# Kernel optimization log

Hardware: AMD Instinct MI355X
Metric: run time of the kernel (lower is better)

## Reference

```python
import jax, jax.numpy as jnp
import numpy as np
from jax import lax

V, E, H, B, S, T = 50000, 256, 512, 16, 400, 100
MAX_OOV, UNK, LAMB = 100, 1, 1.0
NEG = -1e30


def gru_scan(xs, h0, Wih, Whh, bih, bhh):
    """xs: (S,B,E), h0: (B,H) -> (hs (S,B,H), hT (B,H)). PyTorch GRU cell math."""
    gi_all = xs @ Wih.T + bih  # (S,B,3H) precomputed input projections
    def step(h, gi):
        gh = h @ Whh.T + bhh
        r = jax.nn.sigmoid(gi[..., :H] + gh[..., :H])
        z = jax.nn.sigmoid(gi[..., H:2 * H] + gh[..., H:2 * H])
        n = jnp.tanh(gi[..., 2 * H:] + r * gh[..., 2 * H:])
        hn = (1.0 - z) * n + z * h
        return hn, hn
    hT, hs = lax.scan(step, h0, gi_all)
    return hs, hT


def gru_cell(x, h, Wih, Whh, bih, bhh):
    gi = x @ Wih.T + bih
    gh = h @ Whh.T + bhh
    r = jax.nn.sigmoid(gi[..., :H] + gh[..., :H])
    z = jax.nn.sigmoid(gi[..., H:2 * H] + gh[..., H:2 * H])
    n = jnp.tanh(gi[..., 2 * H:] + r * gh[..., 2 * H:])
    return (1.0 - z) * n + z * h


def pgn_forward(floats, src_vecs, tgt_vecs, max_oov):
    (src_mask, enc_embed, dec_embed,
     eWih_f, eWhh_f, ebih_f, ebhh_f, eWih_b, eWhh_b, ebih_b, ebhh_b,
     dWih, dWhh, dbih, dbhh,
     aWh, abh, aWs, abs_, aWc, abc, aV, abv,
     rW, rb, gW, gb, fW, fb) = floats

    # --- encoder (bidirectional GRU) ---
    src_in = jnp.where(src_vecs >= V, UNK, src_vecs)          # replace_oov
    xs = enc_embed[src_in].transpose(1, 0, 2)                  # (S,B,E)
    h0 = jnp.zeros((B, H), xs.dtype)
    hs_f, hT_f = gru_scan(xs, h0, eWih_f, eWhh_f, ebih_f, ebhh_f)
    hs_b, hT_b = gru_scan(xs[::-1], h0, eWih_b, eWhh_b, ebih_b, ebhh_b)
    enc_out = jnp.concatenate([hs_f, hs_b[::-1]], -1).transpose(1, 0, 2)  # (B,S,2H)
    enc_hidden = jnp.concatenate([hT_f, hT_b], -1)             # (B,2H)

    # reducer: initial decoder hidden (torch names it context_vec)
    h_dec0 = enc_hidden @ rW.T + rb                            # (B,H)

    # precompute Wh(enc_output) once (loop-invariant)
    Wh_enc = jnp.einsum('bsd,hd->bsh', enc_out, aWh) + abh     # (B,S,H)
    mask_s = src_mask[..., 0] > 0                              # (B,S)
    wc_vec = aWc[:, 0]                                         # (H,)
    rows = jnp.arange(B)

    dec_in = jnp.where(tgt_vecs[:, :-1] >= V, UNK, tgt_vecs[:, :-1]).T  # (T-1,B)
    targets = tgt_vecs[:, 1:].T                                          # (T-1,B)

    def step(carry, inp):
        h, cov = carry                      # (B,H), (B,S)
        tok, tgt_t = inp
        x = dec_embed[tok]                  # (B,E)
        hdec = gru_cell(x, h, dWih, dWhh, dbih, dbhh)          # (B,H)
        # Bahdanau attention with coverage
        s_part = hdec @ aWs.T + abs_                            # (B,H)
        c_part = cov[:, :, None] * wc_vec[None, None, :] + abc  # (B,S,H)
        e = jnp.tanh(Wh_enc + s_part[:, None, :] + c_part) @ aV[0] + abv[0]  # (B,S)
        attn = jax.nn.softmax(jnp.where(mask_s, e, NEG), axis=1)
        ctx = jnp.einsum('bs,bsd->bd', attn, enc_out)           # (B,2H)
        cov_new = cov + attn
        ctx_red = ctx @ rW.T + rb                               # (B,H)
        logits = jnp.concatenate([ctx_red, hdec], -1) @ fW.T + fb
        p_vocab = jax.nn.softmax(logits, -1)                    # (B,V)
        score = jnp.concatenate([ctx_red, hdec, x], -1) @ gW.T + gb  # (B,1)
        p_gen = jnp.clip(jax.nn.sigmoid(score), 0.001, 0.999)
        p_ext = jnp.concatenate(
            [p_gen * p_vocab, jnp.zeros((B, max_oov), p_vocab.dtype)], 1)
        p_ext = p_ext.at[rows[:, None], src_vecs].add((1.0 - p_gen) * attn)
        tp = p_ext[rows, tgt_t]
        cov_loss = jnp.sum(jnp.minimum(attn, cov_new), axis=1)
        loss = (-jnp.log(tp + 1e-9) + LAMB * cov_loss) * (tgt_t != 0).astype(tp.dtype)
        return (ctx_red, cov_new), loss

    cov0 = jnp.zeros((B, S), enc_out.dtype)
    _, losses = lax.scan(step, (h_dec0, cov0), (dec_in, targets))  # (T-1,B)
    batch_loss = losses.sum(0)
    tgt_lens = jnp.sum((tgt_vecs != 0).astype(batch_loss.dtype), axis=1) - 1.0
    return jnp.mean(batch_loss / tgt_lens)


def setup_inputs() -> dict:
    key = jax.random.key(0)
    ks = iter(jax.random.split(key, 40))
    def p(shape):
        return 0.02 * jax.random.normal(next(ks), shape, dtype=jnp.float32)
    def z(n):
        return jnp.zeros((n,), jnp.float32)
    inp = {
        'src_vecs': jax.random.randint(next(ks), (B, S), 0, V + MAX_OOV),
        'src_mask': jnp.ones((B, S, 1), jnp.float32),
        'tgt_vecs': jax.random.randint(next(ks), (B, T), 0, V),
        'max_oov': MAX_OOV,
        'enc_embed': p((V, E)), 'dec_embed': p((V, E)),
        'eWih_f': p((3 * H, E)), 'eWhh_f': p((3 * H, H)), 'ebih_f': z(3 * H), 'ebhh_f': z(3 * H),
        'eWih_b': p((3 * H, E)), 'eWhh_b': p((3 * H, H)), 'ebih_b': z(3 * H), 'ebhh_b': z(3 * H),
        'dWih': p((3 * H, E)), 'dWhh': p((3 * H, H)), 'dbih': z(3 * H), 'dbhh': z(3 * H),
        'aWh': p((H, 2 * H)), 'abh': z(H), 'aWs': p((H, H)), 'abs_': z(H),
        'aWc': p((H, 1)), 'abc': z(H), 'aV': p((1, H)), 'abv': z(1),
        'rW': p((H, 2 * H)), 'rb': z(H),
        'gW': p((1, 2 * H + E)), 'gb': z(1),
        'fW': p((V, 2 * H)), 'fb': z(V),
    }
    return inp


def reference(src_vecs, src_mask, tgt_vecs, max_oov, enc_embed, dec_embed,
              eWih_f, eWhh_f, ebih_f, ebhh_f, eWih_b, eWhh_b, ebih_b, ebhh_b,
              dWih, dWhh, dbih, dbhh,
              aWh, abh, aWs, abs_, aWc, abc, aV, abv,
              rW, rb, gW, gb, fW, fb):
    floats = (src_mask, enc_embed, dec_embed,
              eWih_f, eWhh_f, ebih_f, ebhh_f, eWih_b, eWhh_b, ebih_b, ebhh_b,
              dWih, dWhh, dbih, dbhh,
              aWh, abh, aWs, abs_, aWc, abc, aV, abv,
              rW, rb, gW, gb, fW, fb)
    return pgn_forward(floats, src_vecs, tgt_vecs, max_oov)
```

## Files before the change

### kernel.cpp

```cpp
#include <hip/hip_runtime.h>

#define V_SZ 50000
#define E_SZ 256
#define H_SZ 512
#define B_SZ 16
#define S_SZ 400
#define T_SZ 100
#define UNK_TOK 1
#define NEGV -1e30f

typedef unsigned short u16;
typedef unsigned int u32;
typedef __attribute__((ext_vector_type(8))) short sv8;
typedef __attribute__((ext_vector_type(4))) float f32x4;

__device__ __forceinline__ float bf2f(u16 u){ return __uint_as_float(((u32)u)<<16); }
__device__ __forceinline__ u16 f2bf(float x){
  u32 u = __float_as_uint(x);
  u32 r = (u + 0x7fffu + ((u>>16)&1u)) >> 16;
  return (u16)r;
}
__device__ __forceinline__ float wsum(float v){
  #pragma unroll
  for (int o=32;o;o>>=1) v += __shfl_xor(v,o);
  return v;
}
__device__ __forceinline__ float wmaxf(float v){
  #pragma unroll
  for (int o=32;o;o>>=1) v = fmaxf(v, __shfl_xor(v,o));
  return v;
}
__device__ __forceinline__ float ftanh(float x){
  float y = fminf(18.f, fmaxf(-18.f, 2.f*x));
  float e = __expf(y);
  return (e-1.f)/(e+1.f);
}
__device__ __forceinline__ float sigf(float x){ return 1.f/(1.f+__expf(-x)); }

__global__ void k_init(u32* h_bf, int* flags, float* cov, float* loss_acc){
  int idx = blockIdx.x*256 + threadIdx.x;
  if (idx < 16384) h_bf[idx] = 0u;
  if (idx < 1024) flags[idx] = 0;
  if (idx < B_SZ*S_SZ) cov[idx] = 0.f;
  if (idx < B_SZ) loss_acc[idx] = 0.f;
}

__global__ void k_transpose(const float* __restrict__ in, float* __restrict__ out, int R, int C){
  __shared__ float t[32][33];
  int c0 = blockIdx.x*32, r0 = blockIdx.y*32;
  int x = threadIdx.x, y = threadIdx.y;
  for (int j=y;j<32;j+=8){
    int r=r0+j, c=c0+x;
    t[j][x] = (r<R && c<C) ? in[r*C+c] : 0.f;
  }
  __syncthreads();
  for (int j=y;j<32;j+=8){
    int oc = c0+j, orr = r0+x;
    if (oc<C && orr<R) out[oc*R+orr] = t[x][j];
  }
}
__global__ void k_f2bf(const float* __restrict__ in, u16* __restrict__ out, int n){
  for (int i = blockIdx.x*256 + threadIdx.x; i < n; i += gridDim.x*256) out[i] = f2bf(in[i]);
}
__global__ void k_prep_frag(const float* __restrict__ W, u16* __restrict__ out, int Nt, int K32, int K){
  int idx = blockIdx.x*256 + threadIdx.x;
  if (idx >= Nt*K32*64) return;
  int lane = idx & 63; int kk = (idx>>6) % K32; int tile = idx / (K32*64);
  const float* src = W + (size_t)(tile*16 + (lane&15))*K + kk*32 + ((lane>>4)<<3);
  u16* dst = out + (size_t)idx*8;
  #pragma unroll
  for (int j=0;j<8;++j) dst[j] = f2bf(src[j]);
}

__global__ void k_gather_src(const int* __restrict__ src, const float* __restrict__ emb, float* __restrict__ xs){
  const int n = S_SZ*B_SZ*E_SZ;
  for (int idx = blockIdx.x*blockDim.x + threadIdx.x; idx < n; idx += gridDim.x*blockDim.x){
    int e = idx & 255; int sb = idx >> 8; int b = sb & 15; int s = sb >> 4;
    int tok = src[b*S_SZ + s]; if (tok >= V_SZ) tok = UNK_TOK;
    xs[idx] = emb[tok*E_SZ + e];
  }
}
__global__ void k_gather_dec(const int* __restrict__ tgt, const float* __restrict__ emb, float* __restrict__ dx){
  const int n = (T_SZ-1)*B_SZ*E_SZ;
  for (int idx = blockIdx.x*blockDim.x + threadIdx.x; idx < n; idx += gridDim.x*blockDim.x){
    int e = idx & 255; int tb = idx >> 8; int b = tb & 15; int t = tb >> 4;
    int tok = tgt[b*T_SZ + t]; if (tok >= V_SZ) tok = UNK_TOK;
    dx[idx] = emb[tok*E_SZ + e];
  }
}
__global__ void k_gxscore(const float* __restrict__ dx, const float* __restrict__ gW, float* __restrict__ gx){
  int i = blockIdx.x*blockDim.x + threadIdx.x;
  if (i < (T_SZ-1)*B_SZ){
    const float* x = dx + i*E_SZ;
    const float* g = gW + 1024;
    float a = 0.f;
    for (int e=0;e<E_SZ;++e) a += x[e]*g[e];
    gx[i] = a;
  }
}

__global__ __launch_bounds__(256) void k_gemm(const float* __restrict__ A, const float* __restrict__ WT,
                       const float* __restrict__ bias, float* __restrict__ C,
                       int M, int N, int K){
  __shared__ float As[32][36];
  int n = blockIdx.x*64 + (threadIdx.x & 63);
  int wv = threadIdx.x >> 6;
  int m0 = blockIdx.y*32;
  float acc[8];
  #pragma unroll
  for (int j=0;j<8;++j) acc[j]=0.f;
  for (int k0=0;k0<K;k0+=32){
    for (int e=threadIdx.x; e<1024; e+=256){
      int r = e>>5, c = e&31;
      int m = m0 + r;
      As[c][r] = (m<M)? A[m*K + k0 + c] : 0.f;
    }
    __syncthreads();
    #pragma unroll 8
    for (int k=0;k<32;++k){
      float w = WT[(k0+k)*N + n];
      const float* as = &As[k][wv*8];
      #pragma unroll
      for (int j=0;j<8;++j) acc[j] += as[j]*w;
    }
    __syncthreads();
  }
  float bv = bias[n];
  #pragma unroll
  for (int j=0;j<8;++j){
    int m = m0 + wv*8 + j;
    if (m<M) C[m*N + n] = acc[j] + bv;
  }
}

__global__ __launch_bounds__(64) void k_enc_persist(
    const float* __restrict__ gi_f, const float* __restrict__ gi_b,
    const u16* __restrict__ Wbf_f, const u16* __restrict__ Wbf_b,
    const float* __restrict__ bhh_f, const float* __restrict__ bhh_b,
    float* __restrict__ enc_out, float* __restrict__ enc_hid,
    u16* __restrict__ h_bf, int* __restrict__ flags){
  __shared__ u16 wl[48*512];
  int lane = threadIdx.x;
  int d = blockIdx.x >> 5, slice = blockIdx.x & 31;
  int h0 = slice*16;
  const u16* Wb = d ? Wbf_b : Wbf_f;
  const float* gi = d ? gi_b : gi_f;
  const float* bhh = d ? bhh_b : bhh_f;
  int hl = h0 + (lane & 15);
  int quad = lane >> 4;
  int* myflag = flags + (d*32 + slice)*16;
  int* pollp  = flags + (d*32 + (lane & 31))*16;

  #pragma unroll 4
  for (int i=0;i<48;++i){
    int gg = i>>4, kk = i&15;
    const u16* src = Wb + ((size_t)(gg*512 + hl))*512 + kk*32 + quad*8;
    *(sv8*)&wl[i*512 + lane*8] = *(const sv8*)src;
  }
  __syncthreads();

  float b0 = bhh[hl], b1 = bhh[512+hl], b2 = bhh[1024+hl];
  float hold[4] = {0.f,0.f,0.f,0.f};

  #pragma unroll 1
  for (int t=0;t<S_SZ;++t){
    int pos = d ? (S_SZ-1-t) : t;
    const float* gp = gi + ((size_t)pos*16)*1536 + hl;
    float giv[12];
    #pragma unroll
    for (int gg=0;gg<3;++gg)
      #pragma unroll
      for (int r=0;r<4;++r)
        giv[gg*4+r] = gp[(quad*4 + r)*1536 + gg*512];

    if (t > 0){
      while (true){
        int v = __hip_atomic_load(pollp, __ATOMIC_RELAXED, __HIP_MEMORY_SCOPE_AGENT);
        unsigned long long m = __ballot(v >= t);
        if (m == ~0ull) break;
        __builtin_amdgcn_s_sleep(1);
      }
      __threadfence();
    }

    const u16* hb = h_bf + ((size_t)(t&1)*2 + d)*8192 + (lane&15)*512 + quad*8;
    f32x4 a0={0.f,0.f,0.f,0.f}, a1={0.f,0.f,0.f,0.f}, a2={0.f,0.f,0.f,0.f};
    #pragma unroll
    for (int kk=0;kk<16;++kk){
      sv8 a = *(const sv8*)(hb + kk*32);
      a0 = __builtin_amdgcn_mfma_f32_16x16x32_bf16(a, *(const sv8*)&wl[(kk)*512 + lane*8], a0, 0,0,0);
      a1 = __builtin_amdgcn_mfma_f32_16x16x32_bf16(a, *(const sv8*)&wl[(16+kk)*512 + lane*8], a1, 0,0,0);
      a2 = __builtin_amdgcn_mfma_f32_16x16x32_bf16(a, *(const sv8*)&wl[(32+kk)*512 + lane*8], a2, 0,0,0);
    }
    u16* hw = h_bf + ((size_t)((t+1)&1)*2 + d)*8192;
    #pragma unroll
    for (int r=0;r<4;++r){
      int b = quad*4 + r;
      float rg = sigf(giv[r]   + a0[r] + b0);
      float zg = sigf(giv[4+r] + a1[r] + b1);
      float ng = ftanh(giv[8+r] + rg*(a2[r] + b2));
      float hv = (1.f-zg)*ng + zg*hold[r];
      hold[r] = hv;
      enc_out[((size_t)b*S_SZ + pos)*1024 + d*512 + hl] = hv;
      hw[b*512 + hl] = f2bf(hv);
      if (t == S_SZ-1) enc_hid[b*1024 + d*512 + hl] = hv;
    }
    __threadfence();
    if (lane == 0)
      __hip_atomic_store(myflag, t+1, __ATOMIC_RELEASE, __HIP_MEMORY_SCOPE_AGENT);
  }
}

__global__ __launch_bounds__(64) void k_dec_mfma(
    const float* __restrict__ dec_gi, u16* __restrict__ u_bf,
    const u16* __restrict__ dfrag, const float* __restrict__ bhh,
    float* __restrict__ hdec, int t){
  int slice = blockIdx.x; int lane = threadIdx.x; int quad = lane >> 4;
  int h = slice*16 + (lane & 15);
  const u16* ap = u_bf + (lane&15)*1024 + quad*8;
  f32x4 a0={0.f,0.f,0.f,0.f}, a1=a0, a2=a0;
  #pragma unroll
  for (int kk=0;kk<16;++kk){
    sv8 a = *(const sv8*)(ap + kk*32);
    a0 = __builtin_amdgcn_mfma_f32_16x16x32_bf16(a, *(const sv8*)(dfrag + ((size_t)(0*32+slice)*16 + kk)*512 + lane*8), a0, 0,0,0);
    a1 = __builtin_amdgcn_mfma_f32_16x16x32_bf16(a, *(const sv8*)(dfrag + ((size_t)(1*32+slice)*16 + kk)*512 + lane*8), a1, 0,0,0);
    a2 = __builtin_amdgcn_mfma_f32_16x16x32_bf16(a, *(const sv8*)(dfrag + ((size_t)(2*32+slice)*16 + kk)*512 + lane*8), a2, 0,0,0);
  }
  float b0 = bhh[h], b1 = bhh[512+h], b2 = bhh[1024+h];
  const float* gi = dec_gi + (size_t)t*16*1536 + h;
  #pragma unroll
  for (int r=0;r<4;++r){
    int b = quad*4 + r;
    const float* gb_ = gi + b*1536;
    float hlv = bf2f(u_bf[b*1024 + h]);
    float rg = sigf(gb_[0]    + a0[r] + b0);
    float zg = sigf(gb_[512]  + a1[r] + b1);
    float ng = ftanh(gb_[1024] + rg*(a2[r] + b2));
    float hv = (1.f-zg)*ng + zg*hlv;
    hdec[b*512 + h] = hv;
    u_bf[b*1024 + 512 + h] = f2bf(hv);
  }
}

__global__ __launch_bounds__(64) void k_spart_mfma(
    const u16* __restrict__ u_bf, const u16* __restrict__ sfrag,
    const float* __restrict__ abs_, float* __restrict__ s_part){
  int slice = blockIdx.x; int lane = threadIdx.x; int quad = lane >> 4;
  const u16* ap = u_bf + (lane&15)*1024 + 512 + quad*8;
  const u16* bp = sfrag + (size_t)slice*16*512 + lane*8;
  f32x4 acc={0.f,0.f,0.f,0.f};
  #pragma unroll
  for (int kk=0;kk<16;++kk){
    sv8 a = *(const sv8*)(ap + kk*32);
    acc = __builtin_amdgcn_mfma_f32_16x16x32_bf16(a, *(const sv8*)(bp + kk*512), acc, 0,0,0);
  }
  int h = slice*16 + (lane & 15);
  float bv = abs_[h];
  #pragma unroll
  for (int r=0;r<4;++r) s_part[(quad*4+r)*512 + h] = acc[r] + bv;
}

__global__ __launch_bounds__(512) void k_escore(
    const float* __restrict__ WhEnc, const float* __restrict__ s_part,
    const float* __restrict__ cov, const float* __restrict__ aWc,
    const float* __restrict__ abc, const float* __restrict__ aV,
    const float* __restrict__ abv, const float* __restrict__ mask,
    float* __restrict__ e_buf){
  int b = blockIdx.x >> 3; int s0 = (blockIdx.x & 7)*50;
  int tid = threadIdx.x, lane = tid & 63, w = tid >> 6;
  __shared__ float sp[512], wc[512], ab[512], av[512];
  sp[tid] = s_part[b*H_SZ + tid];
  wc[tid] = aWc[tid];
  ab[tid] = abc[tid];
  av[tid] = aV[tid];
  __syncthreads();
  float abv0 = abv[0];
  for (int s = s0 + w; s < s0+50; s += 8){
    float cv = cov[b*S_SZ + s];
    const float* wh = WhEnc + (b*S_SZ + s)*H_SZ;
    float a = 0.f;
    #pragma unroll
    for (int j=0;j<8;++j){
      int h = j*64 + lane;
      a += ftanh(wh[h] + sp[h] + cv*wc[h] + ab[h]) * av[h];
    }
    a = wsum(a);
    if (lane == 0){
      float e = a + abv0;
      if (!(mask[b*S_SZ + s] > 0.f)) e = NEGV;
      e_buf[b*S_SZ + s] = e;
    }
  }
}

__global__ __launch_bounds__(512) void k_attn_soft(
    const float* __restrict__ e_buf, float* __restrict__ attn,
    float* __restrict__ cov, float* __restrict__ covloss){
  int b = blockIdx.x; int tid = threadIdx.x, lane = tid & 63, w = tid >> 6;
  __shared__ float red[16];
  float e = (tid < S_SZ) ? e_buf[b*S_SZ + tid] : NEGV;
  float m = wmaxf(e);
  if (lane==0) red[w] = m;
  __syncthreads();
  if (tid < 64){
    float x = (lane < 8) ? red[lane] : NEGV;
    x = wmaxf(x);
    if (lane==0) red[8] = x;
  }
  __syncthreads();
  float mx = red[8];
  float pv = (tid < S_SZ) ? __expf(e - mx) : 0.f;
  float sm = wsum(pv);
  if (lane==0) red[w] = sm;
  __syncthreads();
  if (tid < 64){
    float x = (lane<8)? red[lane] : 0.f;
    x = wsum(x);
    if (lane==0) red[9] = x;
  }
  __syncthreads();
  float inv = 1.f/red[9];
  float ml = 0.f;
  if (tid < S_SZ){
    float a = pv*inv;
    attn[b*S_SZ+tid] = a;
    float cn = cov[b*S_SZ+tid] + a;
    cov[b*S_SZ+tid] = cn;
    ml = fminf(a, cn);
  }
  __syncthreads();
  float cs = wsum(ml);
  if (lane==0) red[w] = cs;
  __syncthreads();
  if (tid==0){
    float tot=0.f;
    for (int i=0;i<8;++i) tot += red[i];
    covloss[b] = tot;
  }
}

__global__ __launch_bounds__(128) void k_ctx(
    const float* __restrict__ attn, const float* __restrict__ enc_out,
    float* __restrict__ ctx){
  int b = blockIdx.x >> 3; int d0 = (blockIdx.x & 7)*128;
  int tid = threadIdx.x;
  float a = 0.f;
  const float* ao = attn + b*S_SZ;
  const float* eo = enc_out + b*S_SZ*1024 + d0 + tid;
  for (int s=0;s<S_SZ;++s) a += ao[s]*eo[s*1024];
  ctx[b*1024 + d0 + tid] = a;
}

__global__ __launch_bounds__(256) void k_ctxred(const float* __restrict__ ctx, const float* __restrict__ rWT,
    const float* __restrict__ rb, float* __restrict__ h_cur, u16* __restrict__ u_bf){
  __shared__ float As[64][17];
  int lane = threadIdx.x & 63, wv = threadIdx.x >> 6;
  int n = blockIdx.x*64 + lane;
  float acc[4] = {0.f,0.f,0.f,0.f};
  for (int k0=0;k0<1024;k0+=64){
    for (int e=threadIdx.x; e<1024; e+=256){
      int r = e & 15, c = e >> 4;
      As[c][r] = ctx[r*1024 + k0 + c];
    }
    __syncthreads();
    #pragma unroll 8
    for (int k=0;k<64;++k){
      float w = rWT[(k0+k)*512 + n];
      #pragma unroll
      for (int j=0;j<4;++j) acc[j] += As[k][wv*4+j]*w;
    }
    __syncthreads();
  }
  float bv = rb[n];
  #pragma unroll
  for (int j=0;j<4;++j){
    int m = wv*4+j;
    float val = acc[j] + bv;
    h_cur[m*512 + n] = val;
    u_bf[m*1024 + n] = f2bf(val);
  }
}

__global__ __launch_bounds__(256) void k_logits_mfma(
    const u16* __restrict__ u_bf, const u16* __restrict__ fwB,
    const float* __restrict__ fb, const int* __restrict__ tgt,
    float* __restrict__ se_part, float* __restrict__ logit_tgt, int t){
  int tid = threadIdx.x, lane = tid & 63, wv = tid >> 6;
  int tile = blockIdx.x*4 + wv;
  bool valid = tile < 3125;
  f32x4 acc = {0.f,0.f,0.f,0.f};
  if (valid){
    const u16* bp = fwB + (size_t)tile*16384 + lane*8;
    const u16* ap = u_bf + (lane&15)*1024 + (lane>>4)*8;
    #pragma unroll 8
    for (int kk=0;kk<32;++kk){
      sv8 a = *(const sv8*)(ap + kk*32);
      sv8 bfr = *(const sv8*)(bp + kk*512);
      acc = __builtin_amdgcn_mfma_f32_16x16x32_bf16(a, bfr, acc, 0,0,0);
    }
  }
  int v = tile*16 + (lane&15);
  float fbv = valid ? fb[v] : 0.f;
  float es0[4];
  #pragma unroll
  for (int r=0;r<4;++r){
    int b = (lane>>4)*4 + r;
    float lg = acc[r] + fbv;
    if (valid && v == tgt[b*T_SZ + t + 1]) logit_tgt[b] = lg;
    es0[r] = valid ? __expf(lg) : 0.f;
  }
  #pragma unroll
  for (int o=1;o<16;o<<=1){
    #pragma unroll
    for (int r=0;r<4;++r) es0[r] += __shfl_xor(es0[r], o);
  }
  __shared__ float part[4][16];
  if ((lane&15)==0){
    #pragma unroll
    for (int r=0;r<4;++r) part[wv][(lane>>4)*4+r] = es0[r];
  }
  __syncthreads();
  if (tid<16) se_part[blockIdx.x*16+tid] = part[0][tid]+part[1][tid]+part[2][tid]+part[3][tid];
}

__global__ __launch_bounds__(256) void k_final(
    const float* __restrict__ attn, const int* __restrict__ src_vecs,
    const int* __restrict__ tgt_vecs, const float* __restrict__ h_cur,
    const float* __restrict__ hdec, const float* __restrict__ gW,
    const float* __restrict__ gb, const float* __restrict__ gx,
    const float* __restrict__ logit_tgt, const float* __restrict__ se_part,
    const float* __restrict__ covloss, float* __restrict__ loss_acc, int t){
  int tid = threadIdx.x, lane = tid&63, w = tid>>6;
  __shared__ float sume[16], pgen[16];
  for (int b = w; b < 16; b += 4){
    float a = 0.f;
    for (int i = lane; i < 782; i += 64) a += se_part[i*16 + b];
    a = wsum(a);
    float dd = 0.f;
    #pragma unroll
    for (int j=0;j<8;++j){
      int k = j*64 + lane;
      dd += h_cur[b*512+k]*gW[k] + hdec[b*512+k]*gW[512+k];
    }
    dd = wsum(dd);
    if (lane==0){
      sume[b] = a;
      float sc = dd + gx[t*B_SZ + b] + gb[0];
      float pg = sigf(sc);
      pgen[b] = fminf(0.999f, fmaxf(0.001f, pg));
    }
  }
  __syncthreads();
  for (int b = w; b < 16; b += 4){
    int tgt = tgt_vecs[b*T_SZ + t + 1];
    float sc = 0.f;
    for (int s = lane; s < S_SZ; s += 64){
      if (src_vecs[b*S_SZ + s] == tgt) sc += attn[b*S_SZ + s];
    }
    sc = wsum(sc);
    if (lane==0){
      float pg = pgen[b];
      float pvv = __expf(logit_tgt[b]) / sume[b];
      float tp = pg*pvv + (1.f-pg)*sc;
      float ls = -logf(tp + 1e-9f) + covloss[b];
      if (tgt != 0) loss_acc[b] += ls;
    }
  }
}

__global__ void k_out(const float* __restrict__ loss_acc, const int* __restrict__ tgt_vecs, float* __restrict__ out){
  __shared__ float s[16];
  int tid = threadIdx.x;
  if (tid < 16){
    int c = 0;
    for (int t=0;t<T_SZ;++t) c += (tgt_vecs[tid*T_SZ + t] != 0) ? 1 : 0;
    s[tid] = loss_acc[tid] / (float)(c - 1);
  }
  __syncthreads();
  if (tid == 0){
    float a = 0.f;
    for (int b=0;b<16;++b) a += s[b];
    out[0] = a / 16.f;
  }
}

extern "C" void kernel_launch(void* const* d_in, const int* in_sizes, int n_in,
                              void* d_out, int out_size, void* d_ws, size_t ws_size,
                              hipStream_t stream){
  (void)in_sizes; (void)n_in; (void)out_size; (void)ws_size;
  const int*   src_vecs = (const int*)d_in[0];
  const float* src_mask = (const float*)d_in[1];
  const int*   tgt_vecs = (const int*)d_in[2];
  const float* enc_embed= (const float*)d_in[4];
  const float* dec_embed= (const float*)d_in[5];
  const float* eWih_f = (const float*)d_in[6];
  const float* eWhh_f = (const float*)d_in[7];
  const float* ebih_f = (const float*)d_in[8];
  const float* ebhh_f = (const float*)d_in[9];
  const float* eWih_b = (const float*)d_in[10];
  const float* eWhh_b = (const float*)d_in[11];
  const float* ebih_b = (const float*)d_in[12];
  const float* ebhh_b = (const float*)d_in[13];
  const float* dWih = (const float*)d_in[14];
  const float* dWhh = (const float*)d_in[15];
  const float* dbih = (const float*)d_in[16];
  const float* dbhh = (const float*)d_in[17];
  const float* aWh  = (const float*)d_in[18];
  const float* abh  = (const float*)d_in[19];
  const float* aWs  = (const float*)d_in[20];
  const float* abs_ = (const float*)d_in[21];
  const float* aWc  = (const float*)d_in[22];
  const float* abc  = (const float*)d_in[23];
  const float* aV   = (const float*)d_in[24];
  const float* abv  = (const float*)d_in[25];
  const float* rW   = (const float*)d_in[26];
  const float* rb   = (const float*)d_in[27];
  const float* gW   = (const float*)d_in[28];
  const float* gb   = (const float*)d_in[29];
  const float* fW   = (const float*)d_in[30];
  const float* fb   = (const float*)d_in[31];
  float* out = (float*)d_out;

  char* p = (char*)d_ws;
  auto alloc = [&](size_t n)->char*{ char* r = p; p += (n + 255) & ~(size_t)255; return r; };
  float* xs      = (float*)alloc((size_t)S_SZ*B_SZ*E_SZ*4);
  float* gi_f    = (float*)alloc((size_t)S_SZ*B_SZ*1536*4);
  float* gi_b    = (float*)alloc((size_t)S_SZ*B_SZ*1536*4);
  float* enc_out = (float*)alloc((size_t)B_SZ*S_SZ*1024*4);
  float* WhEnc   = (float*)alloc((size_t)B_SZ*S_SZ*512*4);
  float* dec_x   = (float*)alloc((size_t)(T_SZ-1)*B_SZ*E_SZ*4);
  float* dec_gi  = (float*)alloc((size_t)(T_SZ-1)*B_SZ*1536*4);
  float* gx      = (float*)alloc((size_t)(T_SZ-1)*B_SZ*4);
  float* eWihT_f = (float*)alloc((size_t)256*1536*4);
  float* eWihT_b = (float*)alloc((size_t)256*1536*4);
  float* dWihT   = (float*)alloc((size_t)256*1536*4);
  float* aWhT    = (float*)alloc((size_t)1024*512*4);
  float* rWT     = (float*)alloc((size_t)1024*512*4);
  u16* Wbf_f     = (u16*)alloc((size_t)1536*512*2);
  u16* Wbf_b     = (u16*)alloc((size_t)1536*512*2);
  u16* dfrag     = (u16*)alloc((size_t)96*16*512*2);
  u16* sfrag     = (u16*)alloc((size_t)32*16*512*2);
  u16* fwB       = (u16*)alloc((size_t)3125*16384*2);
  u16* h_bf      = (u16*)alloc((size_t)2*2*16*512*2);
  u16* u_bf      = (u16*)alloc((size_t)16*1024*2);
  int* flags     = (int*)alloc(64*16*4);
  float* enc_hid = (float*)alloc((size_t)B_SZ*1024*4);
  float* h_cur   = (float*)alloc((size_t)B_SZ*H_SZ*4);
  float* hdec    = (float*)alloc((size_t)B_SZ*H_SZ*4);
  float* s_part  = (float*)alloc((size_t)B_SZ*H_SZ*4);
  float* e_buf   = (float*)alloc((size_t)B_SZ*S_SZ*4);
  float* attn    = (float*)alloc((size_t)B_SZ*S_SZ*4);
  float* cov     = (float*)alloc((size_t)B_SZ*S_SZ*4);
  float* ctx     = (float*)alloc((size_t)B_SZ*1024*4);
  float* se_part = (float*)alloc((size_t)782*16*4);
  float* logit_tgt = (float*)alloc(64*4);
  float* covloss = (float*)alloc(64*4);
  float* loss_acc= (float*)alloc(64*4);

  dim3 tb(32,8);
  k_init<<<128,256,0,stream>>>((u32*)h_bf, flags, cov, loss_acc);
  k_transpose<<<dim3(8,48),tb,0,stream>>>(eWih_f, eWihT_f, 1536, 256);
  k_transpose<<<dim3(8,48),tb,0,stream>>>(eWih_b, eWihT_b, 1536, 256);
  k_transpose<<<dim3(8,48),tb,0,stream>>>(dWih, dWihT, 1536, 256);
  k_transpose<<<dim3(32,16),tb,0,stream>>>(aWh, aWhT, 512, 1024);
  k_transpose<<<dim3(32,16),tb,0,stream>>>(rW, rWT, 512, 1024);
  k_f2bf<<<3072,256,0,stream>>>(eWhh_f, Wbf_f, 1536*512);
  k_f2bf<<<3072,256,0,stream>>>(eWhh_b, Wbf_b, 1536*512);
  k_prep_frag<<<384,256,0,stream>>>(dWhh, dfrag, 96, 16, 512);
  k_prep_frag<<<128,256,0,stream>>>(aWs, sfrag, 32, 16, 512);
  k_prep_frag<<<25000,256,0,stream>>>(fW, fwB, 3125, 32, 1024);
  k_gather_src<<<1024,256,0,stream>>>(src_vecs, enc_embed, xs);
  k_gather_dec<<<512,256,0,stream>>>(tgt_vecs, dec_embed, dec_x);
  k_gxscore<<<7,256,0,stream>>>(dec_x, gW, gx);
  k_gemm<<<dim3(24,200),256,0,stream>>>(xs, eWihT_f, ebih_f, gi_f, 6400,1536,256);
  k_gemm<<<dim3(24,200),256,0,stream>>>(xs, eWihT_b, ebih_b, gi_b, 6400,1536,256);
  k_gemm<<<dim3(24,50),256,0,stream>>>(dec_x, dWihT, dbih, dec_gi, 1584,1536,256);

  k_enc_persist<<<64,64,0,stream>>>(gi_f, gi_b, Wbf_f, Wbf_b, ebhh_f, ebhh_b,
                                    enc_out, enc_hid, h_bf, flags);

  k_ctxred<<<8,256,0,stream>>>(enc_hid, rWT, rb, h_cur, u_bf);
  k_gemm<<<dim3(8,200),256,0,stream>>>(enc_out, aWhT, abh, WhEnc, 6400,512,1024);

  for (int t=0;t<T_SZ-1;++t){
    k_dec_mfma<<<32,64,0,stream>>>(dec_gi, u_bf, dfrag, dbhh, hdec, t);
    k_spart_mfma<<<32,64,0,stream>>>(u_bf, sfrag, abs_, s_part);
    k_escore<<<128,512,0,stream>>>(WhEnc, s_part, cov, aWc, abc, aV, abv, src_mask, e_buf);
    k_attn_soft<<<16,512,0,stream>>>(e_buf, attn, cov, covloss);
    k_ctx<<<128,128,0,stream>>>(attn, enc_out, ctx);
    k_ctxred<<<8,256,0,stream>>>(ctx, rWT, rb, h_cur, u_bf);
    k_logits_mfma<<<782,256,0,stream>>>(u_bf, fwB, fb, tgt_vecs, se_part, logit_tgt, t);
    k_final<<<1,256,0,stream>>>(attn, src_vecs, tgt_vecs, h_cur, hdec, gW, gb, gx,
                                logit_tgt, se_part, covloss, loss_acc, t);
  }
  k_out<<<1,64,0,stream>>>(loss_acc, tgt_vecs, out);
}
```

Before: 18.92 ms.

## Fuse decoder time loop into one persistent kernel with grid barriers

Replaces the eight kernels launched per decoder step with one persistent 256-block kernel that separates the phases using flag-based grid barriers. This removes roughly 800 kernel launches and their gaps. It also pre-multiplies the encoder outputs by the reducer weight, so the context reduction works in the projected 512-dim space (algebraic reassociation). The vocab logits stream weights through LDS with async global_load_lds double buffering, and the loss-finalize phase is overlapped with the next step's GRU. The risks are that the spin barriers need all 256 blocks to be co-resident and that each barrier adds latency.

```diff
diff --git a/kernel.cpp b/kernel.cpp
--- a/kernel.cpp
+++ b/kernel.cpp
@@ -8,6 +8,7 @@
 #define T_SZ 100
 #define UNK_TOK 1
 #define NEGV -1e30f
+#define NB 256
 
 typedef unsigned short u16;
 typedef unsigned int u32;
@@ -37,12 +38,20 @@
 }
 __device__ __forceinline__ float sigf(float x){ return 1.f/(1.f+__expf(-x)); }
 
-__global__ void k_init(u32* h_bf, int* flags, float* cov, float* loss_acc){
+__device__ __forceinline__ void gld16(const u16* g, u16* l){
+  __builtin_amdgcn_global_load_lds((const __attribute__((address_space(1))) void*)g,
+                                   (__attribute__((address_space(3))) void*)l, 16, 0, 0);
+}
+
+__global__ void k_init(u32* h_bf, int* flags, float* cov, float* loss_acc,
+                       int* dflags, float* zeros){
   int idx = blockIdx.x*256 + threadIdx.x;
   if (idx < 16384) h_bf[idx] = 0u;
   if (idx < 1024) flags[idx] = 0;
   if (idx < B_SZ*S_SZ) cov[idx] = 0.f;
-  if (idx < B_SZ) loss_acc[idx] = 0.f;
+  if (idx < 64) loss_acc[idx] = 0.f;
+  if (idx < NB*16) dflags[idx] = 0;
+  if (idx < 512) zeros[idx] = 0.f;
 }
 
 __global__ void k_transpose(const float* __restrict__ in, float* __restrict__ out, int R, int C){
@@ -211,146 +220,6 @@
   }
 }
 
-__global__ __launch_bounds__(64) void k_dec_mfma(
-    const float* __restrict__ dec_gi, u16* __restrict__ u_bf,
-    const u16* __restrict__ dfrag, const float* __restrict__ bhh,
-    float* __restrict__ hdec, int t){
-  int slice = blockIdx.x; int lane = threadIdx.x; int quad = lane >> 4;
-  int h = slice*16 + (lane & 15);
-  const u16* ap = u_bf + (lane&15)*1024 + quad*8;
-  f32x4 a0={0.f,0.f,0.f,0.f}, a1=a0, a2=a0;
-  #pragma unroll
-  for (int kk=0;kk<16;++kk){
-    sv8 a = *(const sv8*)(ap + kk*32);
-    a0 = __builtin_amdgcn_mfma_f32_16x16x32_bf16(a, *(const sv8*)(dfrag + ((size_t)(0*32+slice)*16 + kk)*512 + lane*8), a0, 0,0,0);
-    a1 = __builtin_amdgcn_mfma_f32_16x16x32_bf16(a, *(const sv8*)(dfrag + ((size_t)(1*32+slice)*16 + kk)*512 + lane*8), a1, 0,0,0);
-    a2 = __builtin_amdgcn_mfma_f32_16x16x32_bf16(a, *(const sv8*)(dfrag + ((size_t)(2*32+slice)*16 + kk)*512 + lane*8), a2, 0,0,0);
-  }
-  float b0 = bhh[h], b1 = bhh[512+h], b2 = bhh[1024+h];
-  const float* gi = dec_gi + (size_t)t*16*1536 + h;
-  #pragma unroll
-  for (int r=0;r<4;++r){
-    int b = quad*4 + r;
-    const float* gb_ = gi + b*1536;
-    float hlv = bf2f(u_bf[b*1024 + h]);
-    float rg = sigf(gb_[0]    + a0[r] + b0);
-    float zg = sigf(gb_[512]  + a1[r] + b1);
-    float ng = ftanh(gb_[1024] + rg*(a2[r] + b2));
-    float hv = (1.f-zg)*ng + zg*hlv;
-    hdec[b*512 + h] = hv;
-    u_bf[b*1024 + 512 + h] = f2bf(hv);
-  }
-}
-
-__global__ __launch_bounds__(64) void k_spart_mfma(
-    const u16* __restrict__ u_bf, const u16* __restrict__ sfrag,
-    const float* __restrict__ abs_, float* __restrict__ s_part){
-  int slice = blockIdx.x; int lane = threadIdx.x; int quad = lane >> 4;
-  const u16* ap = u_bf + (lane&15)*1024 + 512 + quad*8;
-  const u16* bp = sfrag + (size_t)slice*16*512 + lane*8;
-  f32x4 acc={0.f,0.f,0.f,0.f};
-  #pragma unroll
-  for (int kk=0;kk<16;++kk){
-    sv8 a = *(const sv8*)(ap + kk*32);
-    acc = __builtin_amdgcn_mfma_f32_16x16x32_bf16(a, *(const sv8*)(bp + kk*512), acc, 0,0,0);
-  }
-  int h = slice*16 + (lane & 15);
-  float bv = abs_[h];
-  #pragma unroll
-  for (int r=0;r<4;++r) s_part[(quad*4+r)*512 + h] = acc[r] + bv;
-}
-
-__global__ __launch_bounds__(512) void k_escore(
-    const float* __restrict__ WhEnc, const float* __restrict__ s_part,
-    const float* __restrict__ cov, const float* __restrict__ aWc,
-    const float* __restrict__ abc, const float* __restrict__ aV,
-    const float* __restrict__ abv, const float* __restrict__ mask,
-    float* __restrict__ e_buf){
-  int b = blockIdx.x >> 3; int s0 = (blockIdx.x & 7)*50;
-  int tid = threadIdx.x, lane = tid & 63, w = tid >> 6;
-  __shared__ float sp[512], wc[512], ab[512], av[512];
-  sp[tid] = s_part[b*H_SZ + tid];
-  wc[tid] = aWc[tid];
-  ab[tid] = abc[tid];
-  av[tid] = aV[tid];
-  __syncthreads();
-  float abv0 = abv[0];
-  for (int s = s0 + w; s < s0+50; s += 8){
-    float cv = cov[b*S_SZ + s];
-    const float* wh = WhEnc + (b*S_SZ + s)*H_SZ;
-    float a = 0.f;
-    #pragma unroll
-    for (int j=0;j<8;++j){
-      int h = j*64 + lane;
-      a += ftanh(wh[h] + sp[h] + cv*wc[h] + ab[h]) * av[h];
-    }
-    a = wsum(a);
-    if (lane == 0){
-      float e = a + abv0;
-      if (!(mask[b*S_SZ + s] > 0.f)) e = NEGV;
-      e_buf[b*S_SZ + s] = e;
-    }
-  }
-}
-
-__global__ __launch_bounds__(512) void k_attn_soft(
-    const float* __restrict__ e_buf, float* __restrict__ attn,
-    float* __restrict__ cov, float* __restrict__ covloss){
-  int b = blockIdx.x; int tid = threadIdx.x, lane = tid & 63, w = tid >> 6;
-  __shared__ float red[16];
-  float e = (tid < S_SZ) ? e_buf[b*S_SZ + tid] : NEGV;
-  float m = wmaxf(e);
-  if (lane==0) red[w] = m;
-  __syncthreads();
-  if (tid < 64){
-    float x = (lane < 8) ? red[lane] : NEGV;
-    x = wmaxf(x);
-    if (lane==0) red[8] = x;
-  }
-  __syncthreads();
-  float mx = red[8];
-  float pv = (tid < S_SZ) ? __expf(e - mx) : 0.f;
-  float sm = wsum(pv);
-  if (lane==0) red[w] = sm;
-  __syncthreads();
-  if (tid < 64){
-    float x = (lane<8)? red[lane] : 0.f;
-    x = wsum(x);
-    if (lane==0) red[9] = x;
-  }
-  __syncthreads();
-  float inv = 1.f/red[9];
-  float ml = 0.f;
-  if (tid < S_SZ){
-    float a = pv*inv;
-    attn[b*S_SZ+tid] = a;
-    float cn = cov[b*S_SZ+tid] + a;
-    cov[b*S_SZ+tid] = cn;
-    ml = fminf(a, cn);
-  }
-  __syncthreads();
-  float cs = wsum(ml);
-  if (lane==0) red[w] = cs;
-  __syncthreads();
-  if (tid==0){
-    float tot=0.f;
-    for (int i=0;i<8;++i) tot += red[i];
-    covloss[b] = tot;
-  }
-}
-
-__global__ __launch_bounds__(128) void k_ctx(
-    const float* __restrict__ attn, const float* __restrict__ enc_out,
-    float* __restrict__ ctx){
-  int b = blockIdx.x >> 3; int d0 = (blockIdx.x & 7)*128;
-  int tid = threadIdx.x;
-  float a = 0.f;
-  const float* ao = attn + b*S_SZ;
-  const float* eo = enc_out + b*S_SZ*1024 + d0 + tid;
-  for (int s=0;s<S_SZ;++s) a += ao[s]*eo[s*1024];
-  ctx[b*1024 + d0 + tid] = a;
-}
-
 __global__ __launch_bounds__(256) void k_ctxred(const float* __restrict__ ctx, const float* __restrict__ rWT,
     const float* __restrict__ rb, float* __restrict__ h_cur, u16* __restrict__ u_bf){
   __shared__ float As[64][17];
@@ -381,90 +250,322 @@
   }
 }
 
-__global__ __launch_bounds__(256) void k_logits_mfma(
-    const u16* __restrict__ u_bf, const u16* __restrict__ fwB,
-    const float* __restrict__ fb, const int* __restrict__ tgt,
-    float* __restrict__ se_part, float* __restrict__ logit_tgt, int t){
-  int tid = threadIdx.x, lane = tid & 63, wv = tid >> 6;
-  int tile = blockIdx.x*4 + wv;
-  bool valid = tile < 3125;
-  f32x4 acc = {0.f,0.f,0.f,0.f};
-  if (valid){
-    const u16* bp = fwB + (size_t)tile*16384 + lane*8;
-    const u16* ap = u_bf + (lane&15)*1024 + (lane>>4)*8;
-    #pragma unroll 8
-    for (int kk=0;kk<32;++kk){
-      sv8 a = *(const sv8*)(ap + kk*32);
-      sv8 bfr = *(const sv8*)(bp + kk*512);
-      acc = __builtin_amdgcn_mfma_f32_16x16x32_bf16(a, bfr, acc, 0,0,0);
-    }
-  }
-  int v = tile*16 + (lane&15);
-  float fbv = valid ? fb[v] : 0.f;
-  float es0[4];
-  #pragma unroll
-  for (int r=0;r<4;++r){
-    int b = (lane>>4)*4 + r;
-    float lg = acc[r] + fbv;
-    if (valid && v == tgt[b*T_SZ + t + 1]) logit_tgt[b] = lg;
-    es0[r] = valid ? __expf(lg) : 0.f;
-  }
-  #pragma unroll
-  for (int o=1;o<16;o<<=1){
+__device__ __forceinline__ void gbar(int* __restrict__ flg, int bi){
+  __syncthreads();
+  if (threadIdx.x == 0){
+    __threadfence();
+    __hip_atomic_store(flg + blockIdx.x*16, bi, __ATOMIC_RELEASE, __HIP_MEMORY_SCOPE_AGENT);
+  }
+  if (threadIdx.x < 64){
+    int i0 = threadIdx.x*4;
+    for (;;){
+      int v0 = __hip_atomic_load(flg + (i0+0)*16, __ATOMIC_RELAXED, __HIP_MEMORY_SCOPE_AGENT);
+      int v1 = __hip_atomic_load(flg + (i0+1)*16, __ATOMIC_RELAXED, __HIP_MEMORY_SCOPE_AGENT);
+      int v2 = __hip_atomic_load(flg + (i0+2)*16, __ATOMIC_RELAXED, __HIP_MEMORY_SCOPE_AGENT);
+      int v3 = __hip_atomic_load(flg + (i0+3)*16, __ATOMIC_RELAXED, __HIP_MEMORY_SCOPE_AGENT);
+      int mn = min(min(v0,v1),min(v2,v3));
+      if (__ballot(mn >= bi) == ~0ull) break;
+      __builtin_amdgcn_s_sleep(1);
+    }
+    __threadfence();
+  }
+  __syncthreads();
+}
+
+__global__ __launch_bounds__(256,2) void k_decoder(
+    const float* __restrict__ dec_gi, u16* __restrict__ u_bf,
+    const u16* __restrict__ dfrag, const u16* __restrict__ sfrag,
+    const float* __restrict__ dbhh, const float* __restrict__ abs_,
+    const float* __restrict__ WhEnc, const float* __restrict__ aWc,
+    const float* __restrict__ abc, const float* __restrict__ aV,
+    const float* __restrict__ abv, const float* __restrict__ mask,
+    const float* __restrict__ encR, const float* __restrict__ rb,
+    const u16* __restrict__ fwB, const float* __restrict__ fb,
+    const int* __restrict__ src_vecs, const int* __restrict__ tgt_vecs,
+    const float* __restrict__ gW, const float* __restrict__ gb,
+    const float* __restrict__ gx,
+    float* __restrict__ hdec2, float* __restrict__ s_part,
+    float* __restrict__ e_buf, float* __restrict__ attn,
+    float* __restrict__ cov, float* __restrict__ ctxp,
+    u16* __restrict__ aFragLo, float* __restrict__ h_cur,
+    float* __restrict__ se_wave, float* __restrict__ logit_tgt,
+    float* __restrict__ covloss, float* __restrict__ loss_acc,
+    int* __restrict__ flg){
+  int tid = threadIdx.x;
+  int lane = tid & 63;
+  int wv = tid >> 6;
+  int blk = blockIdx.x;
+  int gw = blk*4 + wv;
+  int quad = lane >> 4;
+  int bi = 0;
+  float loss_local = 0.f;
+  __shared__ __align__(16) char smem[49152];
+
+  auto phaseH = [&](int tt){
+    int b = blk;
+    float a1 = 0.f, a2v = 0.f, a3 = 0.f;
+    const float* sw = se_wave + b*1024;
     #pragma unroll
-    for (int r=0;r<4;++r) es0[r] += __shfl_xor(es0[r], o);
-  }
-  __shared__ float part[4][16];
-  if ((lane&15)==0){
-    #pragma unroll
-    for (int r=0;r<4;++r) part[wv][(lane>>4)*4+r] = es0[r];
-  }
-  __syncthreads();
-  if (tid<16) se_part[blockIdx.x*16+tid] = part[0][tid]+part[1][tid]+part[2][tid]+part[3][tid];
-}
-
-__global__ __launch_bounds__(256) void k_final(
-    const float* __restrict__ attn, const int* __restrict__ src_vecs,
-    const int* __restrict__ tgt_vecs, const float* __restrict__ h_cur,
-    const float* __restrict__ hdec, const float* __restrict__ gW,
-    const float* __restrict__ gb, const float* __restrict__ gx,
-    const float* __restrict__ logit_tgt, const float* __restrict__ se_part,
-    const float* __restrict__ covloss, float* __restrict__ loss_acc, int t){
-  int tid = threadIdx.x, lane = tid&63, w = tid>>6;
-  __shared__ float sume[16], pgen[16];
-  for (int b = w; b < 16; b += 4){
-    float a = 0.f;
-    for (int i = lane; i < 782; i += 64) a += se_part[i*16 + b];
-    a = wsum(a);
-    float dd = 0.f;
-    #pragma unroll
-    for (int j=0;j<8;++j){
-      int k = j*64 + lane;
-      dd += h_cur[b*512+k]*gW[k] + hdec[b*512+k]*gW[512+k];
-    }
-    dd = wsum(dd);
-    if (lane==0){
-      sume[b] = a;
-      float sc = dd + gx[t*B_SZ + b] + gb[0];
-      float pg = sigf(sc);
-      pgen[b] = fminf(0.999f, fmaxf(0.001f, pg));
-    }
-  }
-  __syncthreads();
-  for (int b = w; b < 16; b += 4){
-    int tgt = tgt_vecs[b*T_SZ + t + 1];
-    float sc = 0.f;
-    for (int s = lane; s < S_SZ; s += 64){
-      if (src_vecs[b*S_SZ + s] == tgt) sc += attn[b*S_SZ + s];
-    }
-    sc = wsum(sc);
-    if (lane==0){
-      float pg = pgen[b];
-      float pvv = __expf(logit_tgt[b]) / sume[b];
-      float tp = pg*pvv + (1.f-pg)*sc;
-      float ls = -logf(tp + 1e-9f) + covloss[b];
-      if (tgt != 0) loss_acc[b] += ls;
-    }
+    for (int i=0;i<4;++i) a1 += sw[tid + i*256];
+    {
+      const float* hc = h_cur + b*512;
+      const float* hd = hdec2 + (size_t)(tt&1)*8192 + b*512;
+      a2v = hc[tid]*gW[tid] + hd[tid]*gW[512+tid]
+          + hc[256+tid]*gW[256+tid] + hd[256+tid]*gW[768+tid];
+    }
+    int tg = tgt_vecs[b*T_SZ + tt + 1];
+    if (src_vecs[b*S_SZ + tid] == tg) a3 += attn[b*S_SZ + tid];
+    if (tid < 144 && src_vecs[b*S_SZ + 256 + tid] == tg) a3 += attn[b*S_SZ + 256 + tid];
+    a1 = wsum(a1); a2v = wsum(a2v); a3 = wsum(a3);
+    float* red = (float*)smem;
+    if (lane == 0){ red[wv] = a1; red[4+wv] = a2v; red[8+wv] = a3; }
+    __syncthreads();
+    if (tid == 0){
+      float sume = red[0]+red[1]+red[2]+red[3];
+      float dd   = red[4]+red[5]+red[6]+red[7];
+      float ptr  = red[8]+red[9]+red[10]+red[11];
+      float sc = dd + gx[tt*16 + b] + gb[0];
+      float pg = fminf(0.999f, fmaxf(0.001f, sigf(sc)));
+      float tp = pg * (__expf(logit_tgt[b]) / sume) + (1.f-pg)*ptr;
+      if (tg != 0) loss_local += -logf(tp + 1e-9f) + covloss[b];
+    }
+    __syncthreads();
+  };
+
+  for (int t = 0; t < T_SZ-1; ++t){
+    if (blk >= 16 && blk < 24){
+      int slice = (blk-16)*4 + wv;
+      int h = slice*16 + (lane & 15);
+      const u16* ap = u_bf + (lane&15)*1024 + quad*8;
+      f32x4 a0={0.f,0.f,0.f,0.f}, a1=a0, a2=a0;
+      #pragma unroll
+      for (int kk=0;kk<16;++kk){
+        sv8 a = *(const sv8*)(ap + kk*32);
+        a0 = __builtin_amdgcn_mfma_f32_16x16x32_bf16(a, *(const sv8*)(dfrag + ((size_t)(0*32+slice)*16 + kk)*512 + lane*8), a0, 0,0,0);
+        a1 = __builtin_amdgcn_mfma_f32_16x16x32_bf16(a, *(const sv8*)(dfrag + ((size_t)(1*32+slice)*16 + kk)*512 + lane*8), a1, 0,0,0);
+        a2 = __builtin_amdgcn_mfma_f32_16x16x32_bf16(a, *(const sv8*)(dfrag + ((size_t)(2*32+slice)*16 + kk)*512 + lane*8), a2, 0,0,0);
+      }
+      float b0 = dbhh[h], b1 = dbhh[512+h], b2 = dbhh[1024+h];
+      const float* gi = dec_gi + (size_t)t*16*1536 + h;
+      float* hd = hdec2 + (size_t)(t&1)*8192;
+      #pragma unroll
+      for (int r=0;r<4;++r){
+        int b = quad*4 + r;
+        const float* gp = gi + b*1536;
+        float hlv = bf2f(u_bf[b*1024 + h]);
+        float rg = sigf(gp[0]    + a0[r] + b0);
+        float zg = sigf(gp[512]  + a1[r] + b1);
+        float ng = ftanh(gp[1024] + rg*(a2[r] + b2));
+        float hv = (1.f-zg)*ng + zg*hlv;
+        hd[b*512 + h] = hv;
+        u_bf[b*1024 + 512 + h] = f2bf(hv);
+      }
+    } else if (blk < 16 && t > 0){
+      phaseH(t-1);
+    }
+    gbar(flg, ++bi);
+
+    if (blk >= 16 && blk < 24){
+      int slice = (blk-16)*4 + wv;
+      const u16* ap = u_bf + (lane&15)*1024 + 512 + quad*8;
+      const u16* bp = sfrag + (size_t)slice*16*512 + lane*8;
+      f32x4 acc={0.f,0.f,0.f,0.f};
+      #pragma unroll
+      for (int kk=0;kk<16;++kk){
+        sv8 a = *(const sv8*)(ap + kk*32);
+        acc = __builtin_amdgcn_mfma_f32_16x16x32_bf16(a, *(const sv8*)(bp + kk*512), acc, 0,0,0);
+      }
+      int h = slice*16 + (lane & 15);
+      float bv = abs_[h];
+      #pragma unroll
+      for (int r=0;r<4;++r) s_part[(quad*4+r)*512 + h] = acc[r] + bv;
+    }
+    gbar(flg, ++bi);
+
+    {
+      float* sp  = (float*)smem;
+      float* wcs = sp + 512;
+      float* abS = sp + 1024;
+      float* avS = sp + 1536;
+      int b = blk >> 4, chunk = blk & 15;
+      for (int i = tid; i < 512; i += 256){
+        sp[i]  = s_part[b*512 + i];
+        wcs[i] = aWc[i];
+        abS[i] = abc[i];
+        avS[i] = aV[i];
+      }
+      __syncthreads();
+      float abv0 = abv[0];
+      int s0 = chunk*25;
+      for (int s = s0 + wv; s < s0 + 25; s += 4){
+        float cv = cov[b*S_SZ + s];
+        const float* wh = WhEnc + (size_t)(b*S_SZ + s)*512;
+        float a = 0.f;
+        #pragma unroll
+        for (int j=0;j<8;++j){
+          int h = j*64 + lane;
+          a += ftanh(wh[h] + sp[h] + cv*wcs[h] + abS[h]) * avS[h];
+        }
+        a = wsum(a);
+        if (lane == 0){
+          float e = a + abv0;
+          if (!(mask[b*S_SZ + s] > 0.f)) e = NEGV;
+          e_buf[b*S_SZ + s] = e;
+        }
+      }
+    }
+    gbar(flg, ++bi);
+
+    if (blk < 16){
+      int b = blk;
+      float* red = (float*)smem;
+      float e0 = e_buf[b*S_SZ + tid];
+      float e1 = (tid < 144) ? e_buf[b*S_SZ + 256 + tid] : NEGV;
+      float m = wmaxf(fmaxf(e0, e1));
+      if (lane == 0) red[wv] = m;
+      __syncthreads();
+      float mx = fmaxf(fmaxf(red[0],red[1]), fmaxf(red[2],red[3]));
+      float p0 = __expf(e0 - mx);
+      float p1 = (tid < 144) ? __expf(e1 - mx) : 0.f;
+      float sm = wsum(p0 + p1);
+      if (lane == 0) red[4+wv] = sm;
+      __syncthreads();
+      float inv = 1.f/(red[4]+red[5]+red[6]+red[7]);
+      float ml;
+      {
+        float a0v = p0*inv;
+        attn[b*S_SZ + tid] = a0v;
+        float cn = cov[b*S_SZ + tid] + a0v;
+        cov[b*S_SZ + tid] = cn;
+        ml = fminf(a0v, cn);
+      }
+      if (tid < 144){
+        float a1v = p1*inv;
+        attn[b*S_SZ + 256 + tid] = a1v;
+        float cn = cov[b*S_SZ + 256 + tid] + a1v;
+        cov[b*S_SZ + 256 + tid] = cn;
+        ml += fminf(a1v, cn);
+      }
+      float cs = wsum(ml);
+      if (lane == 0) red[8+wv] = cs;
+      __syncthreads();
+      if (tid == 0) covloss[b] = red[8]+red[9]+red[10]+red[11];
+    }
+    gbar(flg, ++bi);
+
+    {
+      int b = gw >> 6, rem = gw & 63;
+      int n0 = (rem >> 3) * 64;
+      int q = rem & 7;
+      const float* er = encR + ((size_t)(b*S_SZ) + q*50)*512 + n0 + lane;
+      const float* at = attn + b*S_SZ + q*50;
+      float acc = 0.f;
+      #pragma unroll 5
+      for (int s=0;s<50;++s) acc += at[s] * er[(size_t)s*512];
+      ctxp[(q*16 + b)*512 + n0 + lane] = acc;
+    }
+    gbar(flg, ++bi);
+
+    if (blk < 4){
+      int f = blk*256 + tid;
+      int kk = f >> 6, l = f & 63, r = l & 15;
+      int c8 = ((l >> 4) << 3) + kk*32;
+      float v[8];
+      #pragma unroll
+      for (int j=0;j<8;++j) v[j] = rb[c8+j];
+      #pragma unroll
+      for (int q=0;q<8;++q){
+        const float* pp = ctxp + q*8192 + r*512 + c8;
+        #pragma unroll
+        for (int j=0;j<8;++j) v[j] += pp[j];
+      }
+      sv8 fr;
+      #pragma unroll
+      for (int j=0;j<8;++j) fr[j] = (short)f2bf(v[j]);
+      *(sv8*)&aFragLo[(size_t)f*8] = fr;
+      *(sv8*)&u_bf[r*1024 + c8] = fr;
+      f32x4 v0 = {v[0],v[1],v[2],v[3]};
+      f32x4 v1 = {v[4],v[5],v[6],v[7]};
+      *(f32x4*)&h_cur[r*512 + c8] = v0;
+      *(f32x4*)&h_cur[r*512 + c8 + 4] = v1;
+    }
+    gbar(flg, ++bi);
+
+    {
+      u16* a_lds = (u16*)smem;
+      for (int f = tid; f < 2048; f += 256){
+        sv8 fr;
+        if (f < 1024){
+          fr = *(const sv8*)&aFragLo[(size_t)f*8];
+        } else {
+          int kk = f >> 6, l = f & 63, r = l & 15;
+          int c8 = ((l >> 4) << 3) + kk*32;
+          fr = *(const sv8*)&u_bf[r*1024 + c8];
+        }
+        *(sv8*)&a_lds[(size_t)f*8] = fr;
+      }
+      __syncthreads();
+
+      u16* mybuf = (u16*)(smem + 32768) + wv*2048;
+      int nT = (gw < 53) ? 4 : 3;
+      int nC = nT * 16;
+      int tgtv[4];
+      #pragma unroll
+      for (int r=0;r<4;++r) tgtv[r] = tgt_vecs[(quad*4 + r)*T_SZ + t + 1];
+      float es[4] = {0.f,0.f,0.f,0.f};
+      f32x4 acc = {0.f,0.f,0.f,0.f};
+
+      auto STAGE = [&](int c){
+        int tl = gw + ((c >> 4) << 10);
+        const u16* src = fwB + (size_t)tl*16384 + (size_t)(c & 15)*1024 + lane*8;
+        u16* dst = mybuf + (c & 1)*1024;
+        gld16(src, dst);
+        gld16(src + 512, dst + 512);
+      };
+      STAGE(0); STAGE(1);
+      #pragma unroll 1
+      for (int c = 0; c < nC; ++c){
+        if (c + 1 < nC) { asm volatile("s_waitcnt vmcnt(2)" ::: "memory"); }
+        else            { asm volatile("s_waitcnt vmcnt(0)" ::: "memory"); }
+        const u16* bp = mybuf + (c & 1)*1024 + lane*8;
+        int kk0 = (c & 15)*2;
+        #pragma unroll
+        for (int j=0;j<2;++j){
+          sv8 af  = *(const sv8*)&a_lds[(size_t)(kk0+j)*512 + lane*8];
+          sv8 bfr = *(const sv8*)&bp[j*512];
+          acc = __builtin_amdgcn_mfma_f32_16x16x32_bf16(af, bfr, acc, 0,0,0);
+        }
+        if ((c & 15) == 15){
+          int tl = gw + ((c >> 4) << 10);
+          int v = tl*16 + (lane & 15);
+          float fbv = fb[v];
+          #pragma unroll
+          for (int r=0;r<4;++r){
+            float lg = acc[r] + fbv;
+            if (v == tgtv[r]) logit_tgt[quad*4 + r] = lg;
+            es[r] += __expf(lg);
+          }
+          acc[0]=0.f; acc[1]=0.f; acc[2]=0.f; acc[3]=0.f;
+        }
+        asm volatile("" ::: "memory");
+        if (c + 2 < nC) STAGE(c + 2);
+      }
+      #pragma unroll
+      for (int o=1;o<16;o<<=1){
+        #pragma unroll
+        for (int r=0;r<4;++r) es[r] += __shfl_xor(es[r], o);
+      }
+      if ((lane & 15) == 0){
+        #pragma unroll
+        for (int r=0;r<4;++r) se_wave[(size_t)(quad*4 + r)*1024 + gw] = es[r];
+      }
+    }
+    gbar(flg, ++bi);
+  }
+
+  if (blk < 16){
+    phaseH(T_SZ-2);
+    if (tid == 0) loss_acc[blk] = loss_local;
   }
 }
 
@@ -546,19 +647,23 @@
   int* flags     = (int*)alloc(64*16*4);
   float* enc_hid = (float*)alloc((size_t)B_SZ*1024*4);
   float* h_cur   = (float*)alloc((size_t)B_SZ*H_SZ*4);
-  float* hdec    = (float*)alloc((size_t)B_SZ*H_SZ*4);
   float* s_part  = (float*)alloc((size_t)B_SZ*H_SZ*4);
   float* e_buf   = (float*)alloc((size_t)B_SZ*S_SZ*4);
   float* attn    = (float*)alloc((size_t)B_SZ*S_SZ*4);
   float* cov     = (float*)alloc((size_t)B_SZ*S_SZ*4);
-  float* ctx     = (float*)alloc((size_t)B_SZ*1024*4);
-  float* se_part = (float*)alloc((size_t)782*16*4);
   float* logit_tgt = (float*)alloc(64*4);
   float* covloss = (float*)alloc(64*4);
   float* loss_acc= (float*)alloc(64*4);
+  float* encR    = (float*)alloc((size_t)B_SZ*S_SZ*512*4);
+  float* ctxp    = (float*)alloc((size_t)8*16*512*4);
+  u16* aFragLo   = (u16*)alloc((size_t)1024*8*2);
+  float* se_wave = (float*)alloc((size_t)16*1024*4);
+  float* hdec2   = (float*)alloc((size_t)2*B_SZ*H_SZ*4);
+  int* dflags    = (int*)alloc((size_t)NB*16*4);
+  float* zeros512= (float*)alloc(512*4);
 
   dim3 tb(32,8);
-  k_init<<<128,256,0,stream>>>((u32*)h_bf, flags, cov, loss_acc);
+  k_init<<<128,256,0,stream>>>((u32*)h_bf, flags, cov, loss_acc, dflags, zeros512);
   k_transpose<<<dim3(8,48),tb,0,stream>>>(eWih_f, eWihT_f, 1536, 256);
   k_transpose<<<dim3(8,48),tb,0,stream>>>(eWih_b, eWihT_b, 1536, 256);
   k_transpose<<<dim3(8,48),tb,0,stream>>>(dWih, dWihT, 1536, 256);
@@ -581,17 +686,15 @@
 
   k_ctxred<<<8,256,0,stream>>>(enc_hid, rWT, rb, h_cur, u_bf);
   k_gemm<<<dim3(8,200),256,0,stream>>>(enc_out, aWhT, abh, WhEnc, 6400,512,1024);
-
-  for (int t=0;t<T_SZ-1;++t){
-    k_dec_mfma<<<32,64,0,stream>>>(dec_gi, u_bf, dfrag, dbhh, hdec, t);
-    k_spart_mfma<<<32,64,0,stream>>>(u_bf, sfrag, abs_, s_part);
-    k_escore<<<128,512,0,stream>>>(WhEnc, s_part, cov, aWc, abc, aV, abv, src_mask, e_buf);
-    k_attn_soft<<<16,512,0,stream>>>(e_buf, attn, cov, covloss);
-    k_ctx<<<128,128,0,stream>>>(attn, enc_out, ctx);
-    k_ctxred<<<8,256,0,stream>>>(ctx, rWT, rb, h_cur, u_bf);
-    k_logits_mfma<<<782,256,0,stream>>>(u_bf, fwB, fb, tgt_vecs, se_part, logit_tgt, t);
-    k_final<<<1,256,0,stream>>>(attn, src_vecs, tgt_vecs, h_cur, hdec, gW, gb, gx,
-                                logit_tgt, se_part, covloss, loss_acc, t);
-  }
+  k_gemm<<<dim3(8,200),256,0,stream>>>(enc_out, rWT, zeros512, encR, 6400,512,1024);
+
+  k_decoder<<<NB,256,0,stream>>>(dec_gi, u_bf, dfrag, sfrag, dbhh, abs_,
+                                 WhEnc, aWc, abc, aV, abv, src_mask,
+                                 encR, rb, fwB, fb, src_vecs, tgt_vecs,
+                                 gW, gb, gx,
+                                 hdec2, s_part, e_buf, attn, cov, ctxp,
+                                 aFragLo, h_cur, se_wave, logit_tgt, covloss,
+                                 loss_acc, dflags);
+
   k_out<<<1,64,0,stream>>>(loss_acc, tgt_vecs, out);
 }
```

After: 21.60 ms. 1.14x slower.
